# Optimization experiments

Measured on AMD Instinct MI355X. Metric: run time of the kernel, lower is better.

Reference implementation:

```python
import jax, jax.numpy as jnp
import numpy as np
import math

B_SZ, L, D_MODEL = 2, 2048, 1024
D_STATE, D_CONV, EXPAND = 16, 4, 2
D_INNER = EXPAND * D_MODEL
DT_RANK = math.ceil(D_MODEL / 16)


def setup_inputs() -> dict:
    key = jax.random.key(0)
    ks = jax.random.split(key, 9)
    s = 0.02
    x = jax.random.normal(ks[0], (B_SZ, L, D_MODEL), jnp.float32)
    W_in = jax.random.normal(ks[1], (D_MODEL, 2 * D_INNER), jnp.float32) * s
    conv_w = jax.random.normal(ks[2], (D_INNER, D_CONV), jnp.float32) * 0.1
    conv_b = jax.random.normal(ks[3], (D_INNER,), jnp.float32) * s
    W_xproj = jax.random.normal(ks[4], (D_INNER, DT_RANK + 2 * D_STATE), jnp.float32) * s
    W_dt = jax.random.normal(ks[5], (DT_RANK, D_INNER), jnp.float32) * s
    # dt bias init so softplus(bias) is log-uniform in [dt_min, dt_max]
    dt_min, dt_max = 0.001, 0.1
    dt = jnp.exp(jax.random.uniform(ks[6], (D_INNER,)) * (math.log(dt_max) - math.log(dt_min)) + math.log(dt_min))
    dt = jnp.maximum(dt, 1e-4)
    b_dt = dt + jnp.log(-jnp.expm1(-dt))
    A_log = jnp.log(jnp.broadcast_to(jnp.arange(1, D_STATE + 1, dtype=jnp.float32), (D_INNER, D_STATE)))
    D = jnp.ones((D_INNER,), jnp.float32)
    W_out = jax.random.normal(ks[7], (D_INNER, D_MODEL), jnp.float32) * s
    return {"x": x, "W_in": W_in, "conv_w": conv_w, "conv_b": conv_b,
            "W_xproj": W_xproj, "W_dt": W_dt, "b_dt": b_dt,
            "A_log": A_log, "D": D, "W_out": W_out}


def _silu(v):
    return v * jax.nn.sigmoid(v)


def _mamba_fwd(x, W_in, conv_w, conv_b, W_xproj, W_dt, b_dt, A_log, D, W_out):
    B, Ls, _ = x.shape
    xz = x @ W_in                         # (B, L, 2*d_inner)
    xb, z = jnp.split(xz, 2, axis=-1)
    # causal depthwise conv1d (pad left d_conv-1, truncate to L)
    xp = jnp.pad(xb, ((0, 0), (D_CONV - 1, 0), (0, 0)))
    conv = conv_b
    acc = jnp.zeros_like(xb)
    for k in range(D_CONV):
        acc = acc + xp[:, k:k + Ls, :] * conv_w[:, k]
    xb = _silu(acc + conv_b)
    # input-dependent dt, B, C
    proj = xb @ W_xproj                   # (B, L, dt_rank + 2*d_state)
    dt_in = proj[..., :DT_RANK]
    Bm = proj[..., DT_RANK:DT_RANK + D_STATE]   # (B, L, d_state)
    Cm = proj[..., DT_RANK + D_STATE:]          # (B, L, d_state)
    dt = jax.nn.softplus(dt_in @ W_dt + b_dt)   # (B, L, d_inner)
    A = -jnp.exp(A_log)                         # (d_inner, d_state)

    def step(h, inp):
        x_t, dt_t, B_t, C_t = inp               # (B,d_inner),(B,d_inner),(B,s),(B,s)
        dA = jnp.exp(dt_t[:, :, None] * A)      # (B, d_inner, d_state)
        h = dA * h + (dt_t[:, :, None] * B_t[:, None, :]) * x_t[:, :, None]
        y_t = jnp.einsum('bds,bs->bd', h, C_t)
        return h, y_t

    h0 = jnp.zeros((B, D_INNER, D_STATE), xb.dtype)
    xs = (xb.swapaxes(0, 1), dt.swapaxes(0, 1), Bm.swapaxes(0, 1), Cm.swapaxes(0, 1))
    _, ys = jax.lax.scan(step, h0, xs)          # (L, B, d_inner)
    y = ys.swapaxes(0, 1) + D * xb
    y = y * _silu(z)
    return y @ W_out                            # (B, L, d_model)


def reference(x, W_in, conv_w, conv_b, W_xproj, W_dt, b_dt, A_log, D, W_out):
    return _mamba_fwd(x, W_in, conv_w, conv_b, W_xproj, W_dt, b_dt, A_log, D, W_out)
```

## Files before the change

### kernel.cpp

```cpp
#include <hip/hip_runtime.h>
#include <hip/hip_bf16.h>
#include <math.h>

#define BSZ 2
#define LSEQ 2048
#define DMODEL 1024
#define DSTATE 16
#define DCONV 4
#define DINNER 2048
#define DTRANK 64
#define NPROJ (DTRANK + 2 * DSTATE)
#define NC 32
#define LC 64
#define KS 4
#define KCH (DINNER / KS)
#define TT 8

using short8 = __attribute__((ext_vector_type(8))) short;
using f32x4 = __attribute__((ext_vector_type(4))) float;
using u16x4 = __attribute__((ext_vector_type(4))) unsigned short;

__device__ __forceinline__ float silu_f(float v) {
    return v / (1.f + expf(-v));
}
__device__ __forceinline__ float softplus_f(float v) {
    return fmaxf(v, 0.f) + log1pf(expf(-fabsf(v)));
}
__device__ __forceinline__ unsigned short f2bf(float f) {
    unsigned u = __builtin_bit_cast(unsigned, f);
    u += 0x7fffu + ((u >> 16) & 1u);
    return (unsigned short)(u >> 16);
}
__device__ __forceinline__ float bf2f(unsigned short u) {
    unsigned x = ((unsigned)u) << 16;
    return __builtin_bit_cast(float, x);
}

__device__ __forceinline__ void gld_lds16(const unsigned short* g, unsigned short* l) {
    __builtin_amdgcn_global_load_lds(
        (const __attribute__((address_space(1))) unsigned int*)g,
        (__attribute__((address_space(3))) unsigned int*)l, 16, 0, 0);
}

__device__ __forceinline__ int xcd_swz(int wg, int nwg) {
    return (wg & 7) * (nwg >> 3) + (wg >> 3);
}

__global__ __launch_bounds__(256) void f32_to_bf16_kernel(
    const float* __restrict__ in, unsigned short* __restrict__ out, int n4) {
    int i = blockIdx.x * 256 + threadIdx.x;
    if (i >= n4) return;
    float4 v = reinterpret_cast<const float4*>(in)[i];
    u16x4 o = {f2bf(v.x), f2bf(v.y), f2bf(v.z), f2bf(v.w)};
    reinterpret_cast<u16x4*>(out)[i] = o;
}

__global__ __launch_bounds__(256) void transpose_bf16_kernel(
    const float* __restrict__ in, unsigned short* __restrict__ out, int R, int Cc) {
    __shared__ float t[32][33];
    const int tx = threadIdx.x & 31, ty = threadIdx.x >> 5;
    const int c0 = blockIdx.x * 32, r0 = blockIdx.y * 32;
    for (int i = ty; i < 32; i += 8)
        t[i][tx] = in[(size_t)(r0 + i) * Cc + c0 + tx];
    __syncthreads();
    for (int i = ty; i < 32; i += 8)
        out[(size_t)(c0 + i) * R + r0 + tx] = f2bf(t[tx][i]);
}

template <int EPI, typename CT>
__global__ __launch_bounds__(512) void gemm256(
    const unsigned short* __restrict__ A, const unsigned short* __restrict__ Bt,
    CT* __restrict__ C, CT* __restrict__ C2, int M, int N, int K) {
    extern __shared__ __align__(16) unsigned short lds[];
    unsigned short* As = lds;
    unsigned short* Bs = lds + 3 * 8192;
    const int tid = threadIdx.x;
    const int lane = tid & 63;
    const int w = tid >> 6;
    const int wm = w >> 2, wn = w & 3;
    const int nwg = gridDim.x * gridDim.y;
    const int wg = xcd_swz(blockIdx.y * gridDim.x + blockIdx.x, nwg);
    const int m0 = (wg / gridDim.x) * 256, n0 = (wg % gridDim.x) * 256;
    const int fr = lane & 15, kg = lane >> 4;
    const int kswz = ((kg ^ ((fr >> 1) & 3)) << 3);
    const int srow = tid >> 2;
    const int cs8 = (((tid & 3) ^ ((tid >> 3) & 3)) << 3);
    const int dst = tid * 8;
    const int nt = K / 32;

    f32x4 acc[8][4];
#pragma unroll
    for (int m = 0; m < 8; m++)
#pragma unroll
        for (int n = 0; n < 4; n++) acc[m][n] = (f32x4){0.f, 0.f, 0.f, 0.f};

#define STAGE_A(t)                                                               \
    {                                                                            \
        const int _b = (t) % 3, _k = (t) * 32;                                   \
        gld_lds16(&A[(size_t)(m0 + srow) * K + _k + cs8], &As[_b * 8192 + dst]); \
        gld_lds16(&A[(size_t)(m0 + 128 + srow) * K + _k + cs8],                  \
                  &As[_b * 8192 + dst + 4096]);                                  \
    }
#define STAGE_B(t)                                                               \
    {                                                                            \
        const int _b = (t) % 3, _k = (t) * 32;                                   \
        gld_lds16(&Bt[(size_t)(n0 + srow) * K + _k + cs8], &Bs[_b * 8192 + dst]);\
        gld_lds16(&Bt[(size_t)(n0 + 128 + srow) * K + _k + cs8],                 \
                  &Bs[_b * 8192 + dst + 4096]);                                  \
    }

    STAGE_A(0); STAGE_B(0); STAGE_A(1); STAGE_B(1);
    asm volatile("s_waitcnt vmcnt(4)" ::: "memory");
    __builtin_amdgcn_s_barrier();

    short8 bfr[4];
    for (int t = 0; t < nt; t++) {
        const int buf = t % 3;
        short8 afr[4];
#pragma unroll
        for (int q = 0; q < 4; q++)
            afr[q] = *reinterpret_cast<const short8*>(
                &As[buf * 8192 + (wm * 128 + q * 16 + fr) * 32 + kswz]);
#pragma unroll
        for (int q = 0; q < 4; q++)
            bfr[q] = *reinterpret_cast<const short8*>(
                &Bs[buf * 8192 + (wn * 64 + q * 16 + fr) * 32 + kswz]);
        if (t + 2 < nt) STAGE_A(t + 2);
        __builtin_amdgcn_s_barrier();
        asm volatile("s_waitcnt lgkmcnt(0)" ::: "memory");
        __builtin_amdgcn_sched_barrier(0);
        __builtin_amdgcn_s_setprio(1);
#pragma unroll
        for (int m = 0; m < 4; m++)
#pragma unroll
            for (int n = 0; n < 4; n++)
                acc[m][n] = __builtin_amdgcn_mfma_f32_16x16x32_bf16(
                    afr[m], bfr[n], acc[m][n], 0, 0, 0);
        __builtin_amdgcn_s_setprio(0);
        __builtin_amdgcn_s_barrier();
#pragma unroll
        for (int q = 0; q < 4; q++)
            afr[q] = *reinterpret_cast<const short8*>(
                &As[buf * 8192 + (wm * 128 + 64 + q * 16 + fr) * 32 + kswz]);
        if (t + 2 < nt) STAGE_B(t + 2);
        if (t + 1 < nt) {
            if (t + 2 < nt)
                asm volatile("s_waitcnt vmcnt(4)" ::: "memory");
            else
                asm volatile("s_waitcnt vmcnt(0)" ::: "memory");
        }
        __builtin_amdgcn_s_barrier();
        asm volatile("s_waitcnt lgkmcnt(0)" ::: "memory");
        __builtin_amdgcn_sched_barrier(0);
        __builtin_amdgcn_s_setprio(1);
#pragma unroll
        for (int m = 0; m < 4; m++)
#pragma unroll
            for (int n = 0; n < 4; n++)
                acc[4 + m][n] = __builtin_amdgcn_mfma_f32_16x16x32_bf16(
                    afr[m], bfr[n], acc[4 + m][n], 0, 0, 0);
        __builtin_amdgcn_s_setprio(0);
        __builtin_amdgcn_s_barrier();
    }
#undef STAGE_A
#undef STAGE_B

    const int g4 = kg * 4;
#pragma unroll
    for (int m = 0; m < 8; m++)
#pragma unroll
        for (int n = 0; n < 4; n++)
#pragma unroll
            for (int j = 0; j < 4; j++) {
                int mm = m0 + wm * 128 + m * 16 + g4 + j;
                int nn = n0 + wn * 64 + n * 16 + fr;
                float v = acc[m][n][j];
                if (EPI == 1) {
                    if (nn < DINNER)
                        C[(size_t)mm * DINNER + nn] = f2bf(v);
                    else
                        C2[(size_t)mm * DINNER + (nn - DINNER)] = f2bf(silu_f(v));
                } else {
                    if constexpr (sizeof(CT) == 2)
                        C[(size_t)mm * N + nn] = f2bf(v);
                    else
                        C[(size_t)mm * N + nn] = v;
                }
            }
}

template <int EPI, typename CT>
__global__ __launch_bounds__(256) void gemm_mfma(
    const unsigned short* __restrict__ A, const unsigned short* __restrict__ Bt,
    CT* __restrict__ C, int M, int N, int K) {
    __shared__ __align__(16) unsigned short As[2][4096];
    __shared__ __align__(16) unsigned short Bs[2][4096];
    const int tid = threadIdx.x;
    const int lane = tid & 63;
    const int wid = tid >> 6;
    const int wr = wid >> 1, wc = wid & 1;
    const int nwg = gridDim.x * gridDim.y;
    const int wg = xcd_swz(blockIdx.y * gridDim.x + blockIdx.x, nwg);
    const int m0 = (wg / gridDim.x) * 128, n0 = (wg % gridDim.x) * 128;

    const int r0 = tid >> 2;
    const int r1 = r0 + 64;
    const int d0 = tid * 8;
    const int d1 = d0 + 2048;
    const int cs8 = (((tid & 3) ^ ((tid >> 3) & 3)) << 3);

    f32x4 acc[4][4];
#pragma unroll
    for (int m = 0; m < 4; m++)
#pragma unroll
        for (int n = 0; n < 4; n++) acc[m][n] = (f32x4){0.f, 0.f, 0.f, 0.f};

    const int fr = lane & 15;
    const int kg = lane >> 4;
    const int kswz = ((kg ^ ((fr >> 1) & 3)) << 3);
    const int nt = K / 32;

    gld_lds16(&A[(size_t)(m0 + r0) * K + cs8], &As[0][d0]);
    gld_lds16(&A[(size_t)(m0 + r1) * K + cs8], &As[0][d1]);
    gld_lds16(&Bt[(size_t)(n0 + r0) * K + cs8], &Bs[0][d0]);
    gld_lds16(&Bt[(size_t)(n0 + r1) * K + cs8], &Bs[0][d1]);
    __syncthreads();

    int cur = 0;
    for (int t = 0; t < nt; t++) {
        if (t + 1 < nt) {
            const int k0 = (t + 1) * 32;
            gld_lds16(&A[(size_t)(m0 + r0) * K + k0 + cs8], &As[cur ^ 1][d0]);
            gld_lds16(&A[(size_t)(m0 + r1) * K + k0 + cs8], &As[cur ^ 1][d1]);
            gld_lds16(&Bt[(size_t)(n0 + r0) * K + k0 + cs8], &Bs[cur ^ 1][d0]);
            gld_lds16(&Bt[(size_t)(n0 + r1) * K + k0 + cs8], &Bs[cur ^ 1][d1]);
        }
        short8 a[4], b[4];
#pragma unroll
        for (int m = 0; m < 4; m++)
            a[m] = *reinterpret_cast<const short8*>(
                &As[cur][(wr * 64 + m * 16 + fr) * 32 + kswz]);
#pragma unroll
        for (int n = 0; n < 4; n++)
            b[n] = *reinterpret_cast<const short8*>(
                &Bs[cur][(wc * 64 + n * 16 + fr) * 32 + kswz]);
#pragma unroll
        for (int m = 0; m < 4; m++)
#pragma unroll
            for (int n = 0; n < 4; n++)
                acc[m][n] = __builtin_amdgcn_mfma_f32_16x16x32_bf16(
                    a[m], b[n], acc[m][n], 0, 0, 0);
        __syncthreads();
        cur ^= 1;
    }

    const int g4 = (lane >> 4) * 4;
#pragma unroll
    for (int m = 0; m < 4; m++)
#pragma unroll
        for (int n = 0; n < 4; n++)
#pragma unroll
            for (int j = 0; j < 4; j++) {
                int mm = m0 + wr * 64 + m * 16 + g4 + j;
                int nn = n0 + wc * 64 + n * 16 + fr;
                float v = acc[m][n][j];
                if constexpr (sizeof(CT) == 2)
                    C[(size_t)mm * N + nn] = f2bf(v);
                else
                    C[(size_t)mm * N + nn] = v;
            }
}

__global__ __launch_bounds__(256) void dt_gemm(
    const unsigned short* __restrict__ dtin,
    const unsigned short* __restrict__ WdtT,
    const float* __restrict__ bias,
    unsigned short* __restrict__ dtout) {
    const int lane = threadIdx.x & 63;
    const int wid = threadIdx.x >> 6;
    const int mt = wid >> 1, nh = wid & 1;
    const int m0 = blockIdx.x * 32;
    const int n0 = blockIdx.y * 128 + nh * 64;
    const int fr = lane & 15, kg = lane >> 4;

    f32x4 acc[4];
#pragma unroll
    for (int i = 0; i < 4; i++) acc[i] = (f32x4){0.f, 0.f, 0.f, 0.f};

#pragma unroll
    for (int step = 0; step < 2; step++) {
        short8 a = *reinterpret_cast<const short8*>(
            &dtin[(size_t)(m0 + mt * 16 + fr) * DTRANK + step * 32 + kg * 8]);
#pragma unroll
        for (int nt = 0; nt < 4; nt++) {
            short8 b = *reinterpret_cast<const short8*>(
                &WdtT[(size_t)(n0 + nt * 16 + fr) * DTRANK + step * 32 + kg * 8]);
            acc[nt] = __builtin_amdgcn_mfma_f32_16x16x32_bf16(a, b, acc[nt], 0, 0, 0);
        }
    }
    const int g4 = kg * 4;
#pragma unroll
    for (int nt = 0; nt < 4; nt++)
#pragma unroll
        for (int j = 0; j < 4; j++) {
            int m = m0 + mt * 16 + g4 + j;
            int n = n0 + nt * 16 + fr;
            dtout[(size_t)m * DINNER + n] = f2bf(softplus_f(acc[nt][j] + bias[n]));
        }
}

__global__ __launch_bounds__(256) void proj_splitk(
    const unsigned short* __restrict__ Abf,
    const unsigned short* __restrict__ WxT,
    float* __restrict__ pp) {
    const int lane = threadIdx.x & 63;
    const int wid = threadIdx.x >> 6;
    const int mt = wid >> 1;
    const int nh = wid & 1;
    const int m0 = blockIdx.x * 32;
    const int kc = blockIdx.y;
    const int fr = lane & 15;
    const int kg = lane >> 4;

    const size_t abase = (size_t)(m0 + mt * 16 + fr) * DINNER + kc * KCH + kg * 8;

    f32x4 acc[3];
#pragma unroll
    for (int i = 0; i < 3; i++) acc[i] = (f32x4){0.f, 0.f, 0.f, 0.f};

    for (int step = 0; step < KCH / 32; step++) {
        short8 a = *reinterpret_cast<const short8*>(&Abf[abase + step * 32]);
#pragma unroll
        for (int nt = 0; nt < 3; nt++) {
            int nrow = nh * 48 + nt * 16 + fr;
            short8 b = *reinterpret_cast<const short8*>(
                &WxT[(size_t)nrow * DINNER + kc * KCH + step * 32 + kg * 8]);
            acc[nt] = __builtin_amdgcn_mfma_f32_16x16x32_bf16(a, b, acc[nt], 0, 0, 0);
        }
    }
    const int g4 = (lane >> 4) * 4;
#pragma unroll
    for (int nt = 0; nt < 3; nt++)
#pragma unroll
        for (int j = 0; j < 4; j++) {
            int m = m0 + mt * 16 + g4 + j;
            int n = nh * 48 + nt * 16 + fr;
            pp[((size_t)kc * (BSZ * LSEQ) + m) * NPROJ + n] = acc[nt][j];
        }
}

__global__ __launch_bounds__(256) void proj_reduce(
    const float* __restrict__ pp, float* __restrict__ proj,
    unsigned short* __restrict__ dtin) {
    int i = blockIdx.x * 256 + threadIdx.x;
    if (i >= BSZ * LSEQ * NPROJ) return;
    float s = 0.f;
#pragma unroll
    for (int kc = 0; kc < KS; kc++)
        s += pp[(size_t)kc * BSZ * LSEQ * NPROJ + i];
    proj[i] = s;
    int m = i / NPROJ;
    int n = i - m * NPROJ;
    if (n < DTRANK) dtin[(size_t)m * DTRANK + n] = f2bf(s);
}

__global__ __launch_bounds__(256) void conv_silu_kernel(
    const unsigned short* __restrict__ xin, const float* __restrict__ w,
    const float* __restrict__ bconv, unsigned short* __restrict__ xout) {
    const int tid = threadIdx.x;
    const int d0 = tid * 8;
    const int bt0 = blockIdx.x * TT;
    const int tloc = bt0 & (LSEQ - 1);

    float wk0[8], wk1[8], wk2[8], wk3[8], bb[8];
#pragma unroll
    for (int q = 0; q < 8; q++) {
        float4 wv = *reinterpret_cast<const float4*>(&w[(d0 + q) * 4]);
        wk0[q] = wv.x; wk1[q] = wv.y; wk2[q] = wv.z; wk3[q] = wv.w;
    }
    {
        float4 b0 = *reinterpret_cast<const float4*>(&bconv[d0]);
        float4 b1 = *reinterpret_cast<const float4*>(&bconv[d0 + 4]);
        bb[0] = b0.x; bb[1] = b0.y; bb[2] = b0.z; bb[3] = b0.w;
        bb[4] = b1.x; bb[5] = b1.y; bb[6] = b1.z; bb[7] = b1.w;
    }

    float xm3[8], xm2[8], xm1[8];
    if (tloc >= 3) {
        short8 v3 = *reinterpret_cast<const short8*>(&xin[(size_t)(bt0 - 3) * DINNER + d0]);
        short8 v2 = *reinterpret_cast<const short8*>(&xin[(size_t)(bt0 - 2) * DINNER + d0]);
        short8 v1 = *reinterpret_cast<const short8*>(&xin[(size_t)(bt0 - 1) * DINNER + d0]);
#pragma unroll
        for (int q = 0; q < 8; q++) {
            xm3[q] = bf2f((unsigned short)v3[q]);
            xm2[q] = bf2f((unsigned short)v2[q]);
            xm1[q] = bf2f((unsigned short)v1[q]);
        }
    } else {
#pragma unroll
        for (int q = 0; q < 8; q++) { xm3[q] = 0.f; xm2[q] = 0.f; xm1[q] = 0.f; }
    }

#pragma unroll
    for (int i = 0; i < TT; i++) {
        short8 vc = *reinterpret_cast<const short8*>(&xin[(size_t)(bt0 + i) * DINNER + d0]);
        float xc[8];
        short8 o;
#pragma unroll
        for (int q = 0; q < 8; q++) {
            xc[q] = bf2f((unsigned short)vc[q]);
            float a = bb[q];
            a = fmaf(wk0[q], xm3[q], a);
            a = fmaf(wk1[q], xm2[q], a);
            a = fmaf(wk2[q], xm1[q], a);
            a = fmaf(wk3[q], xc[q], a);
            o[q] = (short)f2bf(silu_f(a));
        }
        *reinterpret_cast<short8*>(&xout[(size_t)(bt0 + i) * DINNER + d0]) = o;
#pragma unroll
        for (int q = 0; q < 8; q++) { xm3[q] = xm2[q]; xm2[q] = xm1[q]; xm1[q] = xc[q]; }
    }
}

__global__ __launch_bounds__(256) void scan_pass1(
    const unsigned short* __restrict__ xb, const unsigned short* __restrict__ dt,
    const float* __restrict__ proj, const float* __restrict__ A_log,
    float* __restrict__ aprod, float* __restrict__ hend) {
    __shared__ float Bs[LC][DSTATE];
    const int tg = blockIdx.x * 256 + threadIdx.x;
    const int d = tg & (DINNER - 1);
    const int bc = tg >> 11;
    const int c = bc & (NC - 1);
    const int b = bc >> 5;

    for (int idx = threadIdx.x; idx < LC * DSTATE; idx += 256) {
        int ti = idx >> 4, j = idx & 15;
        Bs[ti][j] = proj[(size_t)(b * LSEQ + c * LC + ti) * NPROJ + DTRANK + j];
    }
    __syncthreads();

    float Av[DSTATE], h[DSTATE], ap[DSTATE];
#pragma unroll
    for (int s = 0; s < DSTATE; s++) {
        Av[s] = -expf(A_log[d * DSTATE + s]);
        h[s] = 0.f;
        ap[s] = 1.f;
    }

    for (int i = 0; i < LC; i++) {
        size_t base = (size_t)(b * LSEQ + c * LC + i) * DINNER + d;
        float dtv = bf2f(dt[base]);
        float xv = bf2f(xb[base]);
        float dx = dtv * xv;
#pragma unroll
        for (int s = 0; s < DSTATE; s++) {
            float dA = __expf(dtv * Av[s]);
            ap[s] *= dA;
            h[s] = fmaf(dA, h[s], dx * Bs[i][s]);
        }
    }

    size_t o = ((size_t)bc * DINNER + d) * DSTATE;
#pragma unroll
    for (int q = 0; q < 4; q++) {
        *reinterpret_cast<float4*>(&aprod[o + q * 4]) =
            make_float4(ap[4 * q], ap[4 * q + 1], ap[4 * q + 2], ap[4 * q + 3]);
        *reinterpret_cast<float4*>(&hend[o + q * 4]) =
            make_float4(h[4 * q], h[4 * q + 1], h[4 * q + 2], h[4 * q + 3]);
    }
}

__global__ __launch_bounds__(256) void scan_pass2(
    float* __restrict__ aprod, const float* __restrict__ hend) {
    const int tg = blockIdx.x * 256 + threadIdx.x;
    const int s = tg & (DSTATE - 1);
    const int d = (tg >> 4) & (DINNER - 1);
    const int b = tg >> 15;
    float h = 0.f;
    for (int c = 0; c < NC; c++) {
        size_t o = ((size_t)((b * NC + c) * DINNER) + d) * DSTATE + s;
        float a = aprod[o];
        float e = hend[o];
        aprod[o] = h;
        h = fmaf(a, h, e);
    }
}

__global__ __launch_bounds__(256) void scan_pass3(
    const unsigned short* __restrict__ xb, const unsigned short* __restrict__ dt,
    const float* __restrict__ proj, const float* __restrict__ hstart,
    const float* __restrict__ A_log, const float* __restrict__ Dp,
    const unsigned short* __restrict__ sz, unsigned short* __restrict__ ybf) {
    __shared__ float Bs[LC][DSTATE];
    __shared__ float Cs[LC][DSTATE];
    const int tg = blockIdx.x * 256 + threadIdx.x;
    const int d = tg & (DINNER - 1);
    const int bc = tg >> 11;
    const int c = bc & (NC - 1);
    const int b = bc >> 5;

    for (int idx = threadIdx.x; idx < LC * 2 * DSTATE; idx += 256) {
        int ti = idx >> 5, j = idx & 31;
        float v = proj[(size_t)(b * LSEQ + c * LC + ti) * NPROJ + DTRANK + j];
        if (j < DSTATE) Bs[ti][j] = v;
        else            Cs[ti][j - DSTATE] = v;
    }
    __syncthreads();

    float Av[DSTATE], h[DSTATE];
    size_t o = ((size_t)bc * DINNER + d) * DSTATE;
#pragma unroll
    for (int q = 0; q < 4; q++) {
        float4 hv = *reinterpret_cast<const float4*>(&hstart[o + q * 4]);
        h[4 * q] = hv.x; h[4 * q + 1] = hv.y; h[4 * q + 2] = hv.z; h[4 * q + 3] = hv.w;
    }
#pragma unroll
    for (int s = 0; s < DSTATE; s++)
        Av[s] = -expf(A_log[d * DSTATE + s]);
    const float Dd = Dp[d];

    for (int i = 0; i < LC; i++) {
        size_t base = (size_t)(b * LSEQ + c * LC + i) * DINNER + d;
        float dtv = bf2f(dt[base]);
        float xv = bf2f(xb[base]);
        float szv = bf2f(sz[base]);
        float dx = dtv * xv;
        float p = 0.f;
#pragma unroll
        for (int s = 0; s < DSTATE; s++) {
            float dA = __expf(dtv * Av[s]);
            h[s] = fmaf(dA, h[s], dx * Bs[i][s]);
            p = fmaf(h[s], Cs[i][s], p);
        }
        ybf[base] = f2bf((p + Dd * xv) * szv);
    }
}

extern "C" void kernel_launch(void* const* d_in, const int* in_sizes, int n_in,
                              void* d_out, int out_size, void* d_ws,
                              size_t ws_size, hipStream_t stream) {
    const float* x = (const float*)d_in[0];
    const float* W_in = (const float*)d_in[1];
    const float* conv_w = (const float*)d_in[2];
    const float* conv_b = (const float*)d_in[3];
    const float* W_xproj = (const float*)d_in[4];
    const float* W_dt = (const float*)d_in[5];
    const float* b_dt = (const float*)d_in[6];
    const float* A_log = (const float*)d_in[7];
    const float* Dp = (const float*)d_in[8];
    const float* W_out = (const float*)d_in[9];
    float* out = (float*)d_out;

    char* ws = (char*)d_ws;
    const size_t MB = 1u << 20;
    float* pp    = (float*)(ws);
    float* aprod = (float*)(ws);
    float* hend  = (float*)(ws + 8 * MB);
    unsigned short* xbpre_bf = (unsigned short*)(ws + 16 * MB);
    unsigned short* ybf      = (unsigned short*)(ws + 16 * MB);
    unsigned short* sz_bf    = (unsigned short*)(ws + 32 * MB);
    unsigned short* xb_bf    = (unsigned short*)(ws + 48 * MB);
    unsigned short* dt_bf    = (unsigned short*)(ws + 64 * MB);
    float* projbuf           = (float*)(ws + 88 * MB);
    unsigned short* dtin_bf  = (unsigned short*)(ws + 90 * MB);
    unsigned short* xbf      = (unsigned short*)(ws + 91 * MB);
    unsigned short* WinT     = (unsigned short*)(ws + 99 * MB);
    unsigned short* WoutT    = (unsigned short*)(ws + 107 * MB);
    unsigned short* WxT      = (unsigned short*)(ws + 111 * MB);
    unsigned short* WdtT     = (unsigned short*)(ws + 112 * MB);

    const int M = BSZ * LSEQ;
    dim3 blk(256);

    f32_to_bf16_kernel<<<dim3((M * DMODEL / 4 + 255) / 256), blk, 0, stream>>>(
        x, xbf, M * DMODEL / 4);
    transpose_bf16_kernel<<<dim3(2 * DINNER / 32, DMODEL / 32), blk, 0, stream>>>(
        W_in, WinT, DMODEL, 2 * DINNER);
    transpose_bf16_kernel<<<dim3(DMODEL / 32, DINNER / 32), blk, 0, stream>>>(
        W_out, WoutT, DINNER, DMODEL);
    transpose_bf16_kernel<<<dim3(NPROJ / 32, DINNER / 32), blk, 0, stream>>>(
        W_xproj, WxT, DINNER, NPROJ);
    transpose_bf16_kernel<<<dim3(DINNER / 32, DTRANK / 32), blk, 0, stream>>>(
        W_dt, WdtT, DTRANK, DINNER);

    gemm256<1, unsigned short><<<dim3((2 * DINNER) / 256, M / 256), dim3(512),
                                 98304, stream>>>(
        xbf, WinT, xbpre_bf, sz_bf, M, 2 * DINNER, DMODEL);

    conv_silu_kernel<<<dim3(M / TT), blk, 0, stream>>>(
        xbpre_bf, conv_w, conv_b, xb_bf);

    proj_splitk<<<dim3(M / 32, KS), blk, 0, stream>>>(xb_bf, WxT, pp);
    proj_reduce<<<dim3((M * NPROJ) / 256), blk, 0, stream>>>(pp, projbuf, dtin_bf);

    dt_gemm<<<dim3(M / 32, DINNER / 128), blk, 0, stream>>>(
        dtin_bf, WdtT, b_dt, dt_bf);

    const int nthreads1 = BSZ * NC * DINNER;
    scan_pass1<<<dim3(nthreads1 / 256), blk, 0, stream>>>(
        xb_bf, dt_bf, projbuf, A_log, aprod, hend);
    const int nthreads2 = BSZ * DINNER * DSTATE;
    scan_pass2<<<dim3(nthreads2 / 256), blk, 0, stream>>>(aprod, hend);
    scan_pass3<<<dim3(nthreads1 / 256), blk, 0, stream>>>(
        xb_bf, dt_bf, projbuf, aprod, A_log, Dp, sz_bf, ybf);

    gemm_mfma<0, float><<<dim3(DMODEL / 128, M / 128), blk, 0, stream>>>(
        ybf, WoutT, out, M, DMODEL, DINNER);
}
```

Baseline: 270.1 us.

## Fuse prep conversions into one launch and restructure gemm256 to K=64 double-buffered pipeline

Merges the x conversion and four weight-transpose kernels into a single prep kernel that dispatches on block index, removing four launches. Reworks the in-projection GEMM from a triple-buffered K=32 tile into a double-buffered K=64 tile with 8-way XOR swizzle, four interleaved MFMA phases per tile, and staged half-tile prefetches between them, raising LDS to 128KB. The aim is fewer barriers per unit of K and better overlap of global->LDS loads with MFMA work. The cost is higher LDS use, which may limit how many workgroups fit on a CU despite the launch_bounds occupancy hint of 2, along with more complex vmcnt accounting.

```diff
diff --git a/kernel.cpp b/kernel.cpp
--- a/kernel.cpp
+++ b/kernel.cpp
@@ -46,135 +46,195 @@
     return (wg & 7) * (nwg >> 3) + (wg >> 3);
 }
 
-__global__ __launch_bounds__(256) void f32_to_bf16_kernel(
-    const float* __restrict__ in, unsigned short* __restrict__ out, int n4) {
-    int i = blockIdx.x * 256 + threadIdx.x;
-    if (i >= n4) return;
-    float4 v = reinterpret_cast<const float4*>(in)[i];
-    u16x4 o = {f2bf(v.x), f2bf(v.y), f2bf(v.z), f2bf(v.w)};
-    reinterpret_cast<u16x4*>(out)[i] = o;
-}
-
-__global__ __launch_bounds__(256) void transpose_bf16_kernel(
-    const float* __restrict__ in, unsigned short* __restrict__ out, int R, int Cc) {
+__global__ __launch_bounds__(256) void prep_kernel(
+    const float* __restrict__ x, const float* __restrict__ W_in,
+    const float* __restrict__ W_out, const float* __restrict__ W_xproj,
+    const float* __restrict__ W_dt,
+    unsigned short* __restrict__ xbf, unsigned short* __restrict__ WinT,
+    unsigned short* __restrict__ WoutT, unsigned short* __restrict__ WxT,
+    unsigned short* __restrict__ WdtT) {
+    int bid = blockIdx.x;
+    if (bid < 4096) {
+        int i = bid * 256 + threadIdx.x;
+        float4 v = reinterpret_cast<const float4*>(x)[i];
+        u16x4 o = {f2bf(v.x), f2bf(v.y), f2bf(v.z), f2bf(v.w)};
+        reinterpret_cast<u16x4*>(xbf)[i] = o;
+        return;
+    }
+    bid -= 4096;
+    const float* in;
+    unsigned short* outp;
+    int R, Cc, gx;
+    if (bid < 4096) { in = W_in; outp = WinT; R = 1024; Cc = 4096; gx = 128; }
+    else if ((bid -= 4096) < 2048) { in = W_out; outp = WoutT; R = 2048; Cc = 1024; gx = 32; }
+    else if ((bid -= 2048) < 192) { in = W_xproj; outp = WxT; R = 2048; Cc = 96; gx = 3; }
+    else { bid -= 192; in = W_dt; outp = WdtT; R = 64; Cc = 2048; gx = 64; }
+    const int bx = bid % gx, by = bid / gx;
     __shared__ float t[32][33];
     const int tx = threadIdx.x & 31, ty = threadIdx.x >> 5;
-    const int c0 = blockIdx.x * 32, r0 = blockIdx.y * 32;
+    const int c0 = bx * 32, r0 = by * 32;
     for (int i = ty; i < 32; i += 8)
         t[i][tx] = in[(size_t)(r0 + i) * Cc + c0 + tx];
     __syncthreads();
     for (int i = ty; i < 32; i += 8)
-        out[(size_t)(c0 + i) * R + r0 + tx] = f2bf(t[tx][i]);
+        outp[(size_t)(c0 + i) * R + r0 + tx] = f2bf(t[tx][i]);
 }
 
 template <int EPI, typename CT>
-__global__ __launch_bounds__(512) void gemm256(
+__global__ __launch_bounds__(512, 2) void gemm256(
     const unsigned short* __restrict__ A, const unsigned short* __restrict__ Bt,
     CT* __restrict__ C, CT* __restrict__ C2, int M, int N, int K) {
     extern __shared__ __align__(16) unsigned short lds[];
     unsigned short* As = lds;
-    unsigned short* Bs = lds + 3 * 8192;
+    unsigned short* Bs = lds + 32768;
     const int tid = threadIdx.x;
     const int lane = tid & 63;
-    const int w = tid >> 6;
-    const int wm = w >> 2, wn = w & 3;
+    const int w8 = tid >> 6;
+    const int wm = w8 >> 2, wn = w8 & 3;
     const int nwg = gridDim.x * gridDim.y;
     const int wg = xcd_swz(blockIdx.y * gridDim.x + blockIdx.x, nwg);
     const int m0 = (wg / gridDim.x) * 256, n0 = (wg % gridDim.x) * 256;
     const int fr = lane & 15, kg = lane >> 4;
-    const int kswz = ((kg ^ ((fr >> 1) & 3)) << 3);
-    const int srow = tid >> 2;
-    const int cs8 = (((tid & 3) ^ ((tid >> 3) & 3)) << 3);
-    const int dst = tid * 8;
-    const int nt = K / 32;
+    const int s0 = ((kg ^ (fr & 7)) << 3);
+    const int s1 = (((4 + kg) ^ (fr & 7)) << 3);
+    const int cs8 = (((tid & 7) ^ ((tid >> 3) & 7)) << 3);
+    const int srow = tid >> 3;
+    const int nt = K / 64;
 
     f32x4 acc[8][4];
 #pragma unroll
-    for (int m = 0; m < 8; m++)
-#pragma unroll
-        for (int n = 0; n < 4; n++) acc[m][n] = (f32x4){0.f, 0.f, 0.f, 0.f};
-
-#define STAGE_A(t)                                                               \
+    for (int q = 0; q < 8; q++)
+#pragma unroll
+        for (int p = 0; p < 4; p++) acc[q][p] = (f32x4){0.f, 0.f, 0.f, 0.f};
+
+#define SA(tt, h)                                                                \
     {                                                                            \
-        const int _b = (t) % 3, _k = (t) * 32;                                   \
-        gld_lds16(&A[(size_t)(m0 + srow) * K + _k + cs8], &As[_b * 8192 + dst]); \
-        gld_lds16(&A[(size_t)(m0 + 128 + srow) * K + _k + cs8],                  \
-                  &As[_b * 8192 + dst + 4096]);                                  \
-    }
-#define STAGE_B(t)                                                               \
+        const int _b = ((tt) & 1) * 16384, _k = (tt) * 64;                       \
+        gld_lds16(&A[(size_t)(m0 + (h) * 128 + srow) * K + _k + cs8],            \
+                  &As[_b + (((h) * 2) * 512 + tid) * 8]);                        \
+        gld_lds16(&A[(size_t)(m0 + (h) * 128 + 64 + srow) * K + _k + cs8],       \
+                  &As[_b + (((h) * 2 + 1) * 512 + tid) * 8]);                    \
+    }
+#define SB(tt, h)                                                                \
     {                                                                            \
-        const int _b = (t) % 3, _k = (t) * 32;                                   \
-        gld_lds16(&Bt[(size_t)(n0 + srow) * K + _k + cs8], &Bs[_b * 8192 + dst]);\
-        gld_lds16(&Bt[(size_t)(n0 + 128 + srow) * K + _k + cs8],                 \
-                  &Bs[_b * 8192 + dst + 4096]);                                  \
-    }
-
-    STAGE_A(0); STAGE_B(0); STAGE_A(1); STAGE_B(1);
-    asm volatile("s_waitcnt vmcnt(4)" ::: "memory");
+        const int _b = ((tt) & 1) * 16384, _k = (tt) * 64;                       \
+        gld_lds16(&Bt[(size_t)(n0 + (h) * 128 + srow) * K + _k + cs8],           \
+                  &Bs[_b + (((h) * 2) * 512 + tid) * 8]);                        \
+        gld_lds16(&Bt[(size_t)(n0 + (h) * 128 + 64 + srow) * K + _k + cs8],      \
+                  &Bs[_b + (((h) * 2 + 1) * 512 + tid) * 8]);                    \
+    }
+
+    SA(0, 0); SB(0, 0); SB(0, 1); SA(0, 1);
+    asm volatile("s_waitcnt vmcnt(0)" ::: "memory");
     __builtin_amdgcn_s_barrier();
 
-    short8 bfr[4];
+    short8 a[4][2], b[4][2];
     for (int t = 0; t < nt; t++) {
-        const int buf = t % 3;
-        short8 afr[4];
-#pragma unroll
-        for (int q = 0; q < 4; q++)
-            afr[q] = *reinterpret_cast<const short8*>(
-                &As[buf * 8192 + (wm * 128 + q * 16 + fr) * 32 + kswz]);
-#pragma unroll
-        for (int q = 0; q < 4; q++)
-            bfr[q] = *reinterpret_cast<const short8*>(
-                &Bs[buf * 8192 + (wn * 64 + q * 16 + fr) * 32 + kswz]);
-        if (t + 2 < nt) STAGE_A(t + 2);
+        const int bufo = (t & 1) * 16384;
+        const bool pre = (t + 1 < nt);
+#pragma unroll
+        for (int i = 0; i < 4; i++) {
+            const int row = i * 32 + wm * 16 + fr;
+            a[i][0] = *reinterpret_cast<const short8*>(&As[bufo + row * 64 + s0]);
+            a[i][1] = *reinterpret_cast<const short8*>(&As[bufo + row * 64 + s1]);
+        }
+#pragma unroll
+        for (int p = 0; p < 2; p++) {
+            const int row = p * 64 + wn * 16 + fr;
+            b[p][0] = *reinterpret_cast<const short8*>(&Bs[bufo + row * 64 + s0]);
+            b[p][1] = *reinterpret_cast<const short8*>(&Bs[bufo + row * 64 + s1]);
+        }
+        if (pre) SA(t + 1, 0);
         __builtin_amdgcn_s_barrier();
         asm volatile("s_waitcnt lgkmcnt(0)" ::: "memory");
         __builtin_amdgcn_sched_barrier(0);
         __builtin_amdgcn_s_setprio(1);
 #pragma unroll
-        for (int m = 0; m < 4; m++)
-#pragma unroll
-            for (int n = 0; n < 4; n++)
-                acc[m][n] = __builtin_amdgcn_mfma_f32_16x16x32_bf16(
-                    afr[m], bfr[n], acc[m][n], 0, 0, 0);
+        for (int i = 0; i < 4; i++)
+#pragma unroll
+            for (int p = 0; p < 2; p++) {
+                acc[i][p] = __builtin_amdgcn_mfma_f32_16x16x32_bf16(
+                    a[i][0], b[p][0], acc[i][p], 0, 0, 0);
+                acc[i][p] = __builtin_amdgcn_mfma_f32_16x16x32_bf16(
+                    a[i][1], b[p][1], acc[i][p], 0, 0, 0);
+            }
         __builtin_amdgcn_s_setprio(0);
-        __builtin_amdgcn_s_barrier();
-#pragma unroll
-        for (int q = 0; q < 4; q++)
-            afr[q] = *reinterpret_cast<const short8*>(
-                &As[buf * 8192 + (wm * 128 + 64 + q * 16 + fr) * 32 + kswz]);
-        if (t + 2 < nt) STAGE_B(t + 2);
-        if (t + 1 < nt) {
-            if (t + 2 < nt)
-                asm volatile("s_waitcnt vmcnt(4)" ::: "memory");
-            else
-                asm volatile("s_waitcnt vmcnt(0)" ::: "memory");
-        }
+        asm volatile("s_waitcnt vmcnt(4)" ::: "memory");
+        __builtin_amdgcn_s_barrier();
+#pragma unroll
+        for (int p = 2; p < 4; p++) {
+            const int row = p * 64 + wn * 16 + fr;
+            b[p][0] = *reinterpret_cast<const short8*>(&Bs[bufo + row * 64 + s0]);
+            b[p][1] = *reinterpret_cast<const short8*>(&Bs[bufo + row * 64 + s1]);
+        }
+        if (pre) SB(t + 1, 0);
         __builtin_amdgcn_s_barrier();
         asm volatile("s_waitcnt lgkmcnt(0)" ::: "memory");
         __builtin_amdgcn_sched_barrier(0);
         __builtin_amdgcn_s_setprio(1);
 #pragma unroll
-        for (int m = 0; m < 4; m++)
-#pragma unroll
-            for (int n = 0; n < 4; n++)
-                acc[4 + m][n] = __builtin_amdgcn_mfma_f32_16x16x32_bf16(
-                    afr[m], bfr[n], acc[4 + m][n], 0, 0, 0);
+        for (int i = 0; i < 4; i++)
+#pragma unroll
+            for (int p = 2; p < 4; p++) {
+                acc[i][p] = __builtin_amdgcn_mfma_f32_16x16x32_bf16(
+                    a[i][0], b[p][0], acc[i][p], 0, 0, 0);
+                acc[i][p] = __builtin_amdgcn_mfma_f32_16x16x32_bf16(
+                    a[i][1], b[p][1], acc[i][p], 0, 0, 0);
+            }
         __builtin_amdgcn_s_setprio(0);
-        __builtin_amdgcn_s_barrier();
-    }
-#undef STAGE_A
-#undef STAGE_B
+        asm volatile("s_waitcnt vmcnt(4)" ::: "memory");
+        __builtin_amdgcn_s_barrier();
+#pragma unroll
+        for (int i = 0; i < 4; i++) {
+            const int row = (4 + i) * 32 + wm * 16 + fr;
+            a[i][0] = *reinterpret_cast<const short8*>(&As[bufo + row * 64 + s0]);
+            a[i][1] = *reinterpret_cast<const short8*>(&As[bufo + row * 64 + s1]);
+        }
+        if (pre) SB(t + 1, 1);
+        __builtin_amdgcn_s_barrier();
+        asm volatile("s_waitcnt lgkmcnt(0)" ::: "memory");
+        __builtin_amdgcn_sched_barrier(0);
+        __builtin_amdgcn_s_setprio(1);
+#pragma unroll
+        for (int i = 0; i < 4; i++)
+#pragma unroll
+            for (int p = 0; p < 2; p++) {
+                acc[4 + i][p] = __builtin_amdgcn_mfma_f32_16x16x32_bf16(
+                    a[i][0], b[p][0], acc[4 + i][p], 0, 0, 0);
+                acc[4 + i][p] = __builtin_amdgcn_mfma_f32_16x16x32_bf16(
+                    a[i][1], b[p][1], acc[4 + i][p], 0, 0, 0);
+            }
+        __builtin_amdgcn_s_setprio(0);
+        __builtin_amdgcn_s_barrier();
+        if (pre) SA(t + 1, 1);
+        __builtin_amdgcn_s_barrier();
+        __builtin_amdgcn_s_setprio(1);
+#pragma unroll
+        for (int i = 0; i < 4; i++)
+#pragma unroll
+            for (int p = 2; p < 4; p++) {
+                acc[4 + i][p] = __builtin_amdgcn_mfma_f32_16x16x32_bf16(
+                    a[i][0], b[p][0], acc[4 + i][p], 0, 0, 0);
+                acc[4 + i][p] = __builtin_amdgcn_mfma_f32_16x16x32_bf16(
+                    a[i][1], b[p][1], acc[4 + i][p], 0, 0, 0);
+            }
+        __builtin_amdgcn_s_setprio(0);
+        asm volatile("s_waitcnt vmcnt(4)" ::: "memory");
+        __builtin_amdgcn_s_barrier();
+    }
+#undef SA
+#undef SB
 
     const int g4 = kg * 4;
 #pragma unroll
-    for (int m = 0; m < 8; m++)
-#pragma unroll
-        for (int n = 0; n < 4; n++)
+    for (int q = 0; q < 8; q++)
+#pragma unroll
+        for (int p = 0; p < 4; p++)
 #pragma unroll
             for (int j = 0; j < 4; j++) {
-                int mm = m0 + wm * 128 + m * 16 + g4 + j;
-                int nn = n0 + wn * 64 + n * 16 + fr;
-                float v = acc[m][n][j];
+                int mm = m0 + q * 32 + wm * 16 + g4 + j;
+                int nn = n0 + p * 64 + wn * 16 + fr;
+                float v = acc[q][p][j];
                 if (EPI == 1) {
                     if (nn < DINNER)
                         C[(size_t)mm * DINNER + nn] = f2bf(v);
@@ -572,19 +632,11 @@
     const int M = BSZ * LSEQ;
     dim3 blk(256);
 
-    f32_to_bf16_kernel<<<dim3((M * DMODEL / 4 + 255) / 256), blk, 0, stream>>>(
-        x, xbf, M * DMODEL / 4);
-    transpose_bf16_kernel<<<dim3(2 * DINNER / 32, DMODEL / 32), blk, 0, stream>>>(
-        W_in, WinT, DMODEL, 2 * DINNER);
-    transpose_bf16_kernel<<<dim3(DMODEL / 32, DINNER / 32), blk, 0, stream>>>(
-        W_out, WoutT, DINNER, DMODEL);
-    transpose_bf16_kernel<<<dim3(NPROJ / 32, DINNER / 32), blk, 0, stream>>>(
-        W_xproj, WxT, DINNER, NPROJ);
-    transpose_bf16_kernel<<<dim3(DINNER / 32, DTRANK / 32), blk, 0, stream>>>(
-        W_dt, WdtT, DTRANK, DINNER);
+    prep_kernel<<<dim3(4096 + 4096 + 2048 + 192 + 128), blk, 0, stream>>>(
+        x, W_in, W_out, W_xproj, W_dt, xbf, WinT, WoutT, WxT, WdtT);
 
     gemm256<1, unsigned short><<<dim3((2 * DINNER) / 256, M / 256), dim3(512),
-                                 98304, stream>>>(
+                                 131072, stream>>>(
         xbf, WinT, xbpre_bf, sz_bf, M, 2 * DINNER, DMODEL);
 
     conv_silu_kernel<<<dim3(M / TT), blk, 0, stream>>>(
```

Result: faster. 261.2 us (-3.3%).
